# Optimization experiments

Hardware: AMD Instinct MI355X
Metric: run time of the kernel (lower is better)

Reference implementation:

```python
import jax, jax.numpy as jnp
import numpy as np


def setup_inputs() -> dict:
    key = jax.random.key(0)
    ks = jax.random.split(key, 7)
    B, S, D_IN, D_K, D_V = 4, 4096, 1024, 64, 64
    s = 1.0 / np.sqrt(D_IN)
    return {
        "query": jax.random.normal(ks[0], (B, S, D_IN), jnp.float32),
        "key": jax.random.normal(ks[1], (B, S, D_IN), jnp.float32),
        "value": jax.random.normal(ks[2], (B, S, D_IN), jnp.float32),
        "Wq": jax.random.normal(ks[3], (D_IN, D_K), jnp.float32) * s,
        "bq": jnp.zeros((D_K,), jnp.float32),
        "Wk": jax.random.normal(ks[4], (D_IN, D_K), jnp.float32) * s,
        "bk": jnp.zeros((D_K,), jnp.float32),
        "Wv": jax.random.normal(ks[5], (D_IN, D_V), jnp.float32) * s,
        "bv": jnp.zeros((D_V,), jnp.float32),
    }


def reference(query, key, value, Wq, bq, Wk, bk, Wv, bv):
    # q(query) is computed twice in the original but is identical; compute once.
    q = query @ Wq + bq            # [B,S,dk]
    k = key @ Wk + bk              # [B,S,dk]
    v = value @ Wv + bv            # [B,S,dv]
    scale = jnp.asarray(q.shape[-1] ** 0.5, q.dtype)
    scores = jnp.einsum("bqd,bkd->bqk", q, k) / scale  # [B,S,S]
    probs = jax.nn.softmax(scores, axis=-1)
    return jnp.einsum("bqk,bkd->bqd", probs, v)        # [B,S,dv]
```

## Files before the change

### kernel.cpp

```cpp
#include <hip/hip_runtime.h>
#include <cmath>

constexpr int B_  = 4;
constexpr int S_  = 4096;
constexpr int DIN = 1024;
constexpr int DH  = 64;

typedef short bf16x8 __attribute__((ext_vector_type(8)));
typedef float f32x4  __attribute__((ext_vector_type(4)));

#define GPTR(p) (const __attribute__((address_space(1))) unsigned int*)(p)
#define LPTR(p) (__attribute__((address_space(3))) unsigned int*)(p)

__device__ __forceinline__ ushort f2bf(float x) {
    unsigned int u = __float_as_uint(x);
    return (ushort)((u + 0x7FFFu + ((u >> 16) & 1u)) >> 16);
}

__device__ __forceinline__ bf16x8 cvt8(f32x4 a, f32x4 b) {
    union { bf16x8 v; ushort u[8]; } r;
    r.u[0] = f2bf(a[0]); r.u[1] = f2bf(a[1]); r.u[2] = f2bf(a[2]); r.u[3] = f2bf(a[3]);
    r.u[4] = f2bf(b[0]); r.u[5] = f2bf(b[1]); r.u[6] = f2bf(b[2]); r.u[7] = f2bf(b[3]);
    return r.v;
}

#define QSCALE 0.18033688011112042f

__global__ __launch_bounds__(256) void setup_w(
    const float* __restrict__ Wq, const float* __restrict__ Wk,
    const float* __restrict__ Wv, ushort* __restrict__ Wt_g)
{
    const int y = blockIdx.y;
    const float* W = (y == 0) ? Wq : (y == 1) ? Wk : Wv;
    const int g    = blockIdx.x * 256 + threadIdx.x;
    const int lane = g & 63;
    const int nt   = (g >> 6) & 3;
    const int ks   = (g >> 8) & 1;
    const int it   = g >> 9;
    const int m    = lane & 15;
    const int quad = lane >> 4;
    const int n    = nt * 16 + m;
    const int k0   = it * 64 + (ks * 4 + quad) * 8;
    union { uint4 q; ushort u[8]; } r;
    #pragma unroll
    for (int i = 0; i < 8; ++i) r.u[i] = f2bf(W[(size_t)(k0 + i) * DH + n]);
    *(uint4*)(Wt_g + ((size_t)y << 16) + (size_t)g * 8) = r.q;
}

__global__ __launch_bounds__(256, 4) void proj_kernel(
    const float* __restrict__ Xq, const float* __restrict__ Xk, const float* __restrict__ Xv,
    const float* __restrict__ bq, const float* __restrict__ bk, const float* __restrict__ bv,
    const ushort* __restrict__ Wt_g,
    ushort* __restrict__ Qb, ushort* __restrict__ Kb, ushort* __restrict__ Vt)
{
    __shared__ __align__(16) ushort xlds[16384];

    const int y = blockIdx.y;
    const float *X, *bias;
    if (y == 0)      { X = Xq; bias = bq; }
    else if (y == 1) { X = Xk; bias = bk; }
    else             { X = Xv; bias = bv; }

    const int tid  = threadIdx.x;
    const int w    = tid >> 6;
    const int lane = tid & 63;
    const int m    = lane & 15;
    const int quad = lane >> 4;
    const int row0 = blockIdx.x * 16;

    {
        f32x4 va[8], vb[8];
        #pragma unroll
        for (int r = 0; r < 4; ++r) {
            const float* src = X + (size_t)(row0 + w * 4 + r) * DIN + lane * 8;
            #pragma unroll
            for (int sg = 0; sg < 2; ++sg) {
                va[r * 2 + sg] = *(const f32x4*)(src + sg * 512);
                vb[r * 2 + sg] = *(const f32x4*)(src + sg * 512 + 4);
            }
        }
        __builtin_amdgcn_sched_barrier(0);
        #pragma unroll
        for (int r = 0; r < 4; ++r) {
            const int row = w * 4 + r;
            #pragma unroll
            for (int sg = 0; sg < 2; ++sg) {
                const int wi = sg * 8 + (lane >> 3);
                const int fx = (lane & 7) ^ (row & 7);
                *(bf16x8*)&xlds[((wi * 16 + row) * 8 + fx) * 8] =
                    cvt8(va[r * 2 + sg], vb[r * 2 + sg]);
            }
        }
    }
    __syncthreads();

    const float bias_v = bias[w * 16 + m];
    const ushort* wbase = Wt_g + ((size_t)y << 16) + (size_t)(w * 64 + lane) * 8;

    f32x4 acc = {};
    bf16x8 wf0 = *(const bf16x8*)(wbase);
    bf16x8 wf1 = *(const bf16x8*)(wbase + 2048);
    #pragma unroll
    for (int wi = 0; wi < 16; ++wi) {
        bf16x8 nf0 = wf0, nf1 = wf1;
        if (wi < 15) {
            nf0 = *(const bf16x8*)(wbase + (size_t)(wi + 1) * 4096);
            nf1 = *(const bf16x8*)(wbase + (size_t)(wi + 1) * 4096 + 2048);
        }
        const bf16x8 a0 = *(const bf16x8*)&xlds[((wi * 16 + m) * 8 + ( quad      ^ (m & 7))) * 8];
        const bf16x8 a1 = *(const bf16x8*)&xlds[((wi * 16 + m) * 8 + ((4 + quad) ^ (m & 7))) * 8];
        acc = __builtin_amdgcn_mfma_f32_16x16x32_bf16(a0, wf0, acc, 0, 0, 0);
        acc = __builtin_amdgcn_mfma_f32_16x16x32_bf16(a1, wf1, acc, 0, 0, 0);
        wf0 = nf0; wf1 = nf1;
    }

    if (y < 2) {
        ushort* Out = (y == 0) ? Qb : Kb;
        const float sc = (y == 0) ? QSCALE : 1.0f;
        #pragma unroll
        for (int j = 0; j < 4; ++j) {
            const int row = row0 + quad * 4 + j;
            Out[(size_t)row * DH + w * 16 + m] = f2bf((acc[j] + bias_v) * sc);
        }
    } else {
        __syncthreads();
        ushort (*Vx)[32] = (ushort(*)[32])xlds;
        #pragma unroll
        for (int j = 0; j < 4; ++j)
            Vx[w * 16 + m][quad * 4 + j] = f2bf(acc[j] + bias_v);
        __syncthreads();
        const int batch = row0 >> 12;
        const int s0    = row0 & 4095;
        if (tid < 128) {
            const int d = tid >> 1, h = tid & 1;
            const uint4 v = *(const uint4*)&Vx[d][h * 8];
            *(uint4*)(Vt + ((size_t)batch * 64 + d) * S_ + s0 + h * 8) = v;
        }
    }
}

__global__ __launch_bounds__(256, 3) void attn_kernel(
    const ushort* __restrict__ Qb, const ushort* __restrict__ Kb,
    const ushort* __restrict__ Vt, float* __restrict__ Opart, float* __restrict__ Lpart)
{
    __shared__ ushort Ks[2][4096];
    __shared__ ushort Vs[2][4096];
    __shared__ ushort Pt[64 * 72];

    const int tid  = threadIdx.x;
    const int w    = tid >> 6;
    const int lane = tid & 63;
    const int m    = lane & 15;
    const int quad = lane >> 4;
    const int b    = blockIdx.z, jc = blockIdx.y, qt = blockIdx.x;
    const int q0   = qt * 64;

    bf16x8 qf[2];
    #pragma unroll
    for (int ks = 0; ks < 2; ++ks)
        qf[ks] = *(const bf16x8*)(Qb + (size_t)(b * S_ + q0 + w * 16 + m) * 64
                                     + ks * 32 + quad * 8);
    asm volatile("s_waitcnt vmcnt(0)" ::: "memory");
    __builtin_amdgcn_sched_barrier(0);

    f32x4 acc_o[4] = {};
    float Lp[4] = {};

    const ushort* kbase = Kb + (size_t)b * S_ * 64;
    const ushort* vbase = Vt + (size_t)b * 64 * S_;

    auto stage = [&](int jt, int buf) {
        #pragma unroll
        for (int i = 0; i < 2; ++i) {
            const int slot = w * 128 + i * 64 + lane;
            const int j = slot >> 3, c = slot & 7;
            __builtin_amdgcn_global_load_lds(
                GPTR(kbase + (size_t)(jt * 64 + j) * 64 + ((c ^ (j & 7)) * 8)),
                LPTR(&Ks[buf][(w * 128 + i * 64) * 8]), 16, 0, 0);
            __builtin_amdgcn_global_load_lds(
                GPTR(vbase + (size_t)j * S_ + jt * 64 + ((c ^ (j & 7)) * 8)),
                LPTR(&Vs[buf][(w * 128 + i * 64) * 8]), 16, 0, 0);
        }
    };

    stage(jc * 16 + 0, 0);
    stage(jc * 16 + 1, 1);

    for (int it = 0; it < 16; ++it) {
        if (it < 15) asm volatile("s_waitcnt vmcnt(4)" ::: "memory");
        else         asm volatile("s_waitcnt vmcnt(0)" ::: "memory");
        __builtin_amdgcn_sched_barrier(0);
        __builtin_amdgcn_s_barrier();
        __builtin_amdgcn_sched_barrier(0);

        const ushort* ksb = Ks[it & 1];
        const ushort* vsb = Vs[it & 1];

        f32x4 acc_s[4] = {};
        __builtin_amdgcn_s_setprio(1);
        #pragma unroll
        for (int ks = 0; ks < 2; ++ks)
            #pragma unroll
            for (int jt4 = 0; jt4 < 4; ++jt4) {
                const int j = jt4 * 16 + m;
                const bf16x8 kf = *(const bf16x8*)&ksb[j * 64 + (((ks * 4 + quad) ^ (j & 7)) * 8)];
                acc_s[jt4] = __builtin_amdgcn_mfma_f32_16x16x32_bf16(
                    qf[ks], kf, acc_s[jt4], 0, 0, 0);
            }
        __builtin_amdgcn_s_setprio(0);

        #pragma unroll
        for (int jt4 = 0; jt4 < 4; ++jt4)
            #pragma unroll
            for (int r = 0; r < 4; ++r) {
                const float e = exp2f(acc_s[jt4][r]);
                Lp[r] += e;
                Pt[(w * 16 + quad * 4 + r) * 72 + jt4 * 16 + m] = f2bf(e);
            }

        __builtin_amdgcn_s_setprio(1);
        #pragma unroll
        for (int jc2 = 0; jc2 < 2; ++jc2) {
            const bf16x8 pf = *(const bf16x8*)&Pt[(w * 16 + m) * 72 + jc2 * 32 + quad * 8];
            #pragma unroll
            for (int dt = 0; dt < 4; ++dt) {
                const int d = dt * 16 + m;
                const bf16x8 vf = *(const bf16x8*)&vsb[d * 64 + (((jc2 * 4 + quad) ^ (d & 7)) * 8)];
                acc_o[dt] = __builtin_amdgcn_mfma_f32_16x16x32_bf16(pf, vf, acc_o[dt], 0, 0, 0);
            }
        }
        __builtin_amdgcn_s_setprio(0);

        __builtin_amdgcn_sched_barrier(0);
        __builtin_amdgcn_s_barrier();
        __builtin_amdgcn_sched_barrier(0);
        if (it + 2 < 16) stage(jc * 16 + it + 2, it & 1);
    }

    #pragma unroll
    for (int r = 0; r < 4; ++r) {
        float s = Lp[r];
        #pragma unroll
        for (int off = 1; off < 16; off <<= 1)
            s += __shfl_xor(s, off, 64);
        Lp[r] = s;
    }

    const size_t bj = (size_t)(b * 4 + jc);
    float* Ob = Opart + (bj << 18);
    #pragma unroll
    for (int dt = 0; dt < 4; ++dt)
        #pragma unroll
        for (int r = 0; r < 4; ++r) {
            const int row = q0 + w * 16 + quad * 4 + r;
            Ob[(size_t)row * 64 + dt * 16 + m] = acc_o[dt][r];
        }
    if (m == 0) {
        #pragma unroll
        for (int r = 0; r < 4; ++r)
            Lpart[bj * 4096 + q0 + w * 16 + quad * 4 + r] = Lp[r];
    }
}

__global__ __launch_bounds__(256) void reduce_kernel(
    const float* __restrict__ Opart, const float* __restrict__ Lpart, float* __restrict__ out)
{
    const int g    = blockIdx.x * 256 + threadIdx.x;
    const int base = g << 2;
    const int b    = base >> 18;
    const int rem  = base & 0x3FFFF;
    const int q    = rem >> 6;
    float4 o = make_float4(0.f, 0.f, 0.f, 0.f);
    float  l = 0.f;
    #pragma unroll
    for (int jcc = 0; jcc < 4; ++jcc) {
        const float4 p = *(const float4*)(Opart + (((size_t)(b * 4 + jcc)) << 18) + rem);
        o.x += p.x; o.y += p.y; o.z += p.z; o.w += p.w;
        l += Lpart[(size_t)(b * 4 + jcc) * 4096 + q];
    }
    const float inv = 1.0f / l;
    o.x *= inv; o.y *= inv; o.z *= inv; o.w *= inv;
    *(float4*)(out + base) = o;
}

extern "C" void kernel_launch(void* const* d_in, const int* in_sizes, int n_in,
                              void* d_out, int out_size, void* d_ws, size_t ws_size,
                              hipStream_t stream)
{
    const float* query = (const float*)d_in[0];
    const float* key_  = (const float*)d_in[1];
    const float* value = (const float*)d_in[2];
    const float* Wq    = (const float*)d_in[3];
    const float* bq    = (const float*)d_in[4];
    const float* Wk    = (const float*)d_in[5];
    const float* bk    = (const float*)d_in[6];
    const float* Wv    = (const float*)d_in[7];
    const float* bv    = (const float*)d_in[8];
    float* out = (float*)d_out;

    char* ws = (char*)d_ws;
    ushort* Qb    = (ushort*)(ws);
    ushort* Kb    = (ushort*)(ws + (2  << 20));
    ushort* Vt    = (ushort*)(ws + (4  << 20));
    float*  Opart = (float*) (ws + (6  << 20));
    float*  Lpart = (float*) (ws + (22 << 20));
    ushort* Wt_g  = (ushort*)(ws + (6  << 20));

    setup_w<<<dim3(32, 3), 256, 0, stream>>>(Wq, Wk, Wv, Wt_g);
    proj_kernel<<<dim3(1024, 3), 256, 0, stream>>>(
        query, key_, value, bq, bk, bv, Wt_g, Qb, Kb, Vt);
    attn_kernel<<<dim3(64, 4, 4), 256, 0, stream>>>(Qb, Kb, Vt, Opart, Lpart);
    reduce_kernel<<<dim3(1024), 256, 0, stream>>>(Opart, Lpart, out);
}
```

Measured before the change: 257.8 us.

## Fuse split-K reduction into attention kernel using two in-block key groups

The attention kernel now runs 512-thread blocks, one per query tile and batch. The two 4-wave groups each handle half of the keys. Partial outputs and row sums are combined through shared memory, and the normalized result is written straight to the output. This removes the separate reduce kernel and the global Opart/Lpart round trip, which also drops the s_setprio hints. In exchange the grid shrinks to 256 blocks at one block per CU, lowering wave occupancy and latency hiding compared with the previous 1024-block, 3-per-CU launch.

```diff
diff --git a/kernel.cpp b/kernel.cpp
--- a/kernel.cpp
+++ b/kernel.cpp
@@ -139,26 +139,30 @@
     }
 }
 
-__global__ __launch_bounds__(256, 3) void attn_kernel(
+__global__ __launch_bounds__(512, 1) void attn_kernel(
     const ushort* __restrict__ Qb, const ushort* __restrict__ Kb,
-    const ushort* __restrict__ Vt, float* __restrict__ Opart, float* __restrict__ Lpart)
+    const ushort* __restrict__ Vt, float* __restrict__ out)
 {
-    __shared__ ushort Ks[2][4096];
-    __shared__ ushort Vs[2][4096];
-    __shared__ ushort Pt[64 * 72];
+    __shared__ ushort Ks[2][2][4096];
+    __shared__ ushort Vs[2][2][4096];
+    __shared__ ushort Pt[128 * 72];
+    __shared__ float  Osc[64][68];
+    __shared__ float  Lsc[64];
 
     const int tid  = threadIdx.x;
     const int w    = tid >> 6;
+    const int wg   = w & 3;
+    const int g    = w >> 2;
     const int lane = tid & 63;
     const int m    = lane & 15;
     const int quad = lane >> 4;
-    const int b    = blockIdx.z, jc = blockIdx.y, qt = blockIdx.x;
+    const int b    = blockIdx.y, qt = blockIdx.x;
     const int q0   = qt * 64;
 
     bf16x8 qf[2];
     #pragma unroll
     for (int ks = 0; ks < 2; ++ks)
-        qf[ks] = *(const bf16x8*)(Qb + (size_t)(b * S_ + q0 + w * 16 + m) * 64
+        qf[ks] = *(const bf16x8*)(Qb + (size_t)(b * S_ + q0 + wg * 16 + m) * 64
                                      + ks * 32 + quad * 8);
     asm volatile("s_waitcnt vmcnt(0)" ::: "memory");
     __builtin_amdgcn_sched_barrier(0);
@@ -172,32 +176,31 @@
     auto stage = [&](int jt, int buf) {
         #pragma unroll
         for (int i = 0; i < 2; ++i) {
-            const int slot = w * 128 + i * 64 + lane;
+            const int slot = wg * 128 + i * 64 + lane;
             const int j = slot >> 3, c = slot & 7;
             __builtin_amdgcn_global_load_lds(
                 GPTR(kbase + (size_t)(jt * 64 + j) * 64 + ((c ^ (j & 7)) * 8)),
-                LPTR(&Ks[buf][(w * 128 + i * 64) * 8]), 16, 0, 0);
+                LPTR(&Ks[g][buf][(wg * 128 + i * 64) * 8]), 16, 0, 0);
             __builtin_amdgcn_global_load_lds(
                 GPTR(vbase + (size_t)j * S_ + jt * 64 + ((c ^ (j & 7)) * 8)),
-                LPTR(&Vs[buf][(w * 128 + i * 64) * 8]), 16, 0, 0);
+                LPTR(&Vs[g][buf][(wg * 128 + i * 64) * 8]), 16, 0, 0);
         }
     };
 
-    stage(jc * 16 + 0, 0);
-    stage(jc * 16 + 1, 1);
-
-    for (int it = 0; it < 16; ++it) {
-        if (it < 15) asm volatile("s_waitcnt vmcnt(4)" ::: "memory");
+    stage(g * 32 + 0, 0);
+    stage(g * 32 + 1, 1);
+
+    for (int it = 0; it < 32; ++it) {
+        if (it < 31) asm volatile("s_waitcnt vmcnt(4)" ::: "memory");
         else         asm volatile("s_waitcnt vmcnt(0)" ::: "memory");
         __builtin_amdgcn_sched_barrier(0);
         __builtin_amdgcn_s_barrier();
         __builtin_amdgcn_sched_barrier(0);
 
-        const ushort* ksb = Ks[it & 1];
-        const ushort* vsb = Vs[it & 1];
+        const ushort* ksb = Ks[g][it & 1];
+        const ushort* vsb = Vs[g][it & 1];
 
         f32x4 acc_s[4] = {};
-        __builtin_amdgcn_s_setprio(1);
         #pragma unroll
         for (int ks = 0; ks < 2; ++ks)
             #pragma unroll
@@ -207,7 +210,6 @@
                 acc_s[jt4] = __builtin_amdgcn_mfma_f32_16x16x32_bf16(
                     qf[ks], kf, acc_s[jt4], 0, 0, 0);
             }
-        __builtin_amdgcn_s_setprio(0);
 
         #pragma unroll
         for (int jt4 = 0; jt4 < 4; ++jt4)
@@ -218,7 +220,6 @@
                 Pt[(w * 16 + quad * 4 + r) * 72 + jt4 * 16 + m] = f2bf(e);
             }
 
-        __builtin_amdgcn_s_setprio(1);
         #pragma unroll
         for (int jc2 = 0; jc2 < 2; ++jc2) {
             const bf16x8 pf = *(const bf16x8*)&Pt[(w * 16 + m) * 72 + jc2 * 32 + quad * 8];
@@ -229,12 +230,11 @@
                 acc_o[dt] = __builtin_amdgcn_mfma_f32_16x16x32_bf16(pf, vf, acc_o[dt], 0, 0, 0);
             }
         }
-        __builtin_amdgcn_s_setprio(0);
 
         __builtin_amdgcn_sched_barrier(0);
         __builtin_amdgcn_s_barrier();
         __builtin_amdgcn_sched_barrier(0);
-        if (it + 2 < 16) stage(jc * 16 + it + 2, it & 1);
+        if (it + 2 < 32) stage(g * 32 + it + 2, it & 1);
     }
 
     #pragma unroll
@@ -246,41 +246,31 @@
         Lp[r] = s;
     }
 
-    const size_t bj = (size_t)(b * 4 + jc);
-    float* Ob = Opart + (bj << 18);
-    #pragma unroll
-    for (int dt = 0; dt < 4; ++dt)
+    if (g == 1) {
+        #pragma unroll
+        for (int dt = 0; dt < 4; ++dt)
+            #pragma unroll
+            for (int r = 0; r < 4; ++r)
+                Osc[wg * 16 + quad * 4 + r][dt * 16 + m] = acc_o[dt][r];
+        if (m == 0) {
+            #pragma unroll
+            for (int r = 0; r < 4; ++r)
+                Lsc[wg * 16 + quad * 4 + r] = Lp[r];
+        }
+    }
+    __syncthreads();
+    if (g == 0) {
+        float* Ob = out + ((size_t)b * S_ + q0) * DH;
         #pragma unroll
         for (int r = 0; r < 4; ++r) {
-            const int row = q0 + w * 16 + quad * 4 + r;
-            Ob[(size_t)row * 64 + dt * 16 + m] = acc_o[dt][r];
-        }
-    if (m == 0) {
-        #pragma unroll
-        for (int r = 0; r < 4; ++r)
-            Lpart[bj * 4096 + q0 + w * 16 + quad * 4 + r] = Lp[r];
-    }
-}
-
-__global__ __launch_bounds__(256) void reduce_kernel(
-    const float* __restrict__ Opart, const float* __restrict__ Lpart, float* __restrict__ out)
-{
-    const int g    = blockIdx.x * 256 + threadIdx.x;
-    const int base = g << 2;
-    const int b    = base >> 18;
-    const int rem  = base & 0x3FFFF;
-    const int q    = rem >> 6;
-    float4 o = make_float4(0.f, 0.f, 0.f, 0.f);
-    float  l = 0.f;
-    #pragma unroll
-    for (int jcc = 0; jcc < 4; ++jcc) {
-        const float4 p = *(const float4*)(Opart + (((size_t)(b * 4 + jcc)) << 18) + rem);
-        o.x += p.x; o.y += p.y; o.z += p.z; o.w += p.w;
-        l += Lpart[(size_t)(b * 4 + jcc) * 4096 + q];
-    }
-    const float inv = 1.0f / l;
-    o.x *= inv; o.y *= inv; o.z *= inv; o.w *= inv;
-    *(float4*)(out + base) = o;
+            const int row = wg * 16 + quad * 4 + r;
+            const float inv = 1.0f / (Lp[r] + Lsc[row]);
+            #pragma unroll
+            for (int dt = 0; dt < 4; ++dt)
+                Ob[(size_t)row * DH + dt * 16 + m] =
+                    (acc_o[dt][r] + Osc[row][dt * 16 + m]) * inv;
+        }
+    }
 }
 
 extern "C" void kernel_launch(void* const* d_in, const int* in_sizes, int n_in,
@@ -299,16 +289,13 @@
     float* out = (float*)d_out;
 
     char* ws = (char*)d_ws;
-    ushort* Qb    = (ushort*)(ws);
-    ushort* Kb    = (ushort*)(ws + (2  << 20));
-    ushort* Vt    = (ushort*)(ws + (4  << 20));
-    float*  Opart = (float*) (ws + (6  << 20));
-    float*  Lpart = (float*) (ws + (22 << 20));
-    ushort* Wt_g  = (ushort*)(ws + (6  << 20));
+    ushort* Qb   = (ushort*)(ws);
+    ushort* Kb   = (ushort*)(ws + (2 << 20));
+    ushort* Vt   = (ushort*)(ws + (4 << 20));
+    ushort* Wt_g = (ushort*)(ws + (6 << 20));
 
     setup_w<<<dim3(32, 3), 256, 0, stream>>>(Wq, Wk, Wv, Wt_g);
     proj_kernel<<<dim3(1024, 3), 256, 0, stream>>>(
         query, key_, value, bq, bk, bv, Wt_g, Qb, Kb, Vt);
-    attn_kernel<<<dim3(64, 4, 4), 256, 0, stream>>>(Qb, Kb, Vt, Opart, Lpart);
-    reduce_kernel<<<dim3(1024), 256, 0, stream>>>(Opart, Lpart, out);
-}
+    attn_kernel<<<dim3(64, 4), 512, 0, stream>>>(Qb, Kb, Vt, out);
+}
```

New measurement: 258.3 us. About the same (+0.2%).
